# Performance work log

Hardware: AMD Instinct MI355X
Metric: run time of the kernel (lower is better)

Reference implementation:

```python
import jax, jax.numpy as jnp
import numpy as np

T, B, I, H = 129, 1024, 512, 2048


def setup_inputs() -> dict:
    key = jax.random.key(0)
    ks = jax.random.split(key, 12)
    s = 1.0 / np.sqrt(H)  # torch RNNCell/Linear default U(-1/sqrt(H), 1/sqrt(H))

    def u(k, shape):
        return jax.random.uniform(k, shape, jnp.float32, -s, s)

    x = jax.random.normal(ks[0], (T, B, I), jnp.float32)
    return {
        "x": x,
        "enc_Wih": u(ks[1], (H, I)), "enc_Whh": u(ks[2], (H, H)),
        "enc_bih": u(ks[3], (H,)),   "enc_bhh": u(ks[4], (H,)),
        "dec_Wih": u(ks[5], (H, I)), "dec_Whh": u(ks[6], (H, H)),
        "dec_bih": u(ks[7], (H,)),   "dec_bhh": u(ks[8], (H,)),
        "ro_W": u(ks[9], (I, H)),    "ro_b": u(ks[10], (I,)),
    }


def reference(x, enc_Wih, enc_Whh, enc_bih, enc_bhh,
              dec_Wih, dec_Whh, dec_bih, dec_bhh, ro_W, ro_b):
    T_, B_, I_ = x.shape
    H_ = enc_Whh.shape[0]
    k = (T_ - 3) // 2

    # ---- encode: k+2 RNNCell steps over x[0:k+2] ----
    def enc_step(h, xt):
        h = jnp.tanh(xt @ enc_Wih.T + enc_bih + h @ enc_Whh.T + enc_bhh)
        return h, None

    h0 = jnp.zeros((B_, H_), x.dtype)
    h, _ = jax.lax.scan(enc_step, h0, x[:k + 2])

    # begin_char: one-hot at index 0 (also the default fill of `outputs`)
    begin = jnp.zeros((B_, I_), x.dtype).at[:, 0].set(1.0)

    # ---- decode: k+1 steps, input is zeros (so zeros @ dec_Wih == 0) ----
    def dec_step(carry, _):
        h, done = carry
        h = jnp.tanh(dec_bih + h @ dec_Whh.T + dec_bhh)
        out = jax.nn.log_softmax(h @ ro_W.T + ro_b, axis=1)  # [B, I]
        z = (jnp.argmax(out, axis=1) == 2).astype(x.dtype)
        done = jnp.maximum(done, z)
        b = done[:, None]
        o = (1.0 - b) * out + b * begin
        return (h, done), o

    done0 = jnp.zeros((B_,), x.dtype)
    (_, _), outputs = jax.lax.scan(dec_step, (h, done0), None, length=k + 1)
    return outputs  # [k+1, B, I]
```

## Files before the change

kernel.cpp:

```cpp
#include <hip/hip_runtime.h>
#include <math.h>

constexpr int Bsz  = 1024;
constexpr int Isz  = 512;
constexpr int Hsz  = 2048;
constexpr int Tenc = 65;
constexpr int Tdec = 64;
constexpr int BI   = Bsz * Isz;
constexpr int MNh  = Bsz * Hsz;

typedef _Float16 half8 __attribute__((ext_vector_type(8)));
typedef float    f32x4 __attribute__((ext_vector_type(4)));
typedef unsigned int uint;
typedef unsigned short ushort;

__device__ inline uint pack_split(float v) {
    _Float16 a0 = (_Float16)v;
    float r = (v - (float)a0) * 4096.f;
    _Float16 a1 = (_Float16)r;
    return ((uint)__builtin_bit_cast(ushort, a1) << 16) | __builtin_bit_cast(ushort, a0);
}

struct U8 { uint4 a, b; };
__device__ inline U8 ld8(const uint* __restrict__ p) {
    U8 r; r.a = *(const uint4*)p; r.b = *(const uint4*)(p + 4); return r;
}

__device__ inline void split8(const U8& v, half8& lo, half8& hi) {
    union { uint4 u; float f[4]; } A, B;
    A.u = v.a; B.u = v.b;
    float x[8] = {A.f[0], A.f[1], A.f[2], A.f[3], B.f[0], B.f[1], B.f[2], B.f[3]};
#pragma unroll
    for (int e = 0; e < 8; ++e) {
        _Float16 a0 = (_Float16)x[e];
        float r = (x[e] - (float)a0) * 4096.f;
        lo[e] = a0; hi[e] = (_Float16)r;
    }
}

__device__ inline void unpack8(const U8& v, half8& lo, half8& hi) {
    union { uint u[4]; half8 h; } L, H;
    uint w[8] = {v.a.x, v.a.y, v.a.z, v.a.w, v.b.x, v.b.y, v.b.z, v.b.w};
#pragma unroll
    for (int q = 0; q < 4; ++q) {
        L.u[q] = __builtin_amdgcn_perm(w[2*q+1], w[2*q], 0x05040100u);
        H.u[q] = __builtin_amdgcn_perm(w[2*q+1], w[2*q], 0x07060302u);
    }
    lo = L.h; hi = H.h;
}

__device__ __forceinline__ void gll16(const uint* g, uint* l) {
    __builtin_amdgcn_global_load_lds(
        (const __attribute__((address_space(1))) void*)(uintptr_t)g,
        (__attribute__((address_space(3))) void*)(unsigned int)(uintptr_t)l,
        16, 0, 0);
}

__device__ __forceinline__ void gemm_body(
    uint* ldsA, uint* ldsB,
    const uint* A1, int K1, const uint* B1,
    const uint* A2, int K2, const uint* B2,
    float* P, int M, int N, int GM, int GN, int KS, int bid)
{
    constexpr int NV = 8;
    const int tid  = threadIdx.x;
    const int wid  = tid >> 6, lane = tid & 63;
    const int wr   = wid >> 1, wc = wid & 1;
    const int kq   = lane >> 4, lr = lane & 15;

    const int xcd = bid & 7, g = bid >> 3;
    int n_b, m_b, ks;
    const int spx = GN >> 3;
    if (spx > 0) {
        n_b = xcd * spx + (g % spx);
        int r = g / spx; m_b = r % GM; ks = r / GM;
    } else {
        const int xpn = 8 / GN;
        n_b = xcd / xpn;
        int r = g * xpn + (xcd % xpn); m_b = r % GM; ks = r / GM;
    }
    const int m0 = m_b * 128, n0 = n_b * 128;

    int offA1[4], offA2[4], offB1[4], offB2[4];
#pragma unroll
    for (int q = 0; q < 4; ++q) {
        int U = q * 256 + tid, row = U >> 3, us = U & 7;
        int u = us ^ (row & 7);
        offA1[q] = (m0 + row) * K1 + u * 4;
        offA2[q] = (m0 + row) * K2 + u * 4;
        offB1[q] = (n0 + row) * K1 + u * 4;
        offB2[q] = (n0 + row) * K2 + u * 4;
    }
    const int ldsbase = wid * 256;

    const int R1 = K1 / 32;
    const int R  = (K1 + K2) / 32;
    const int nr = R / KS;
    const int r0 = ks * nr;

    auto STAGE = [&](int r, int bi) {
        uint* Ab = ldsA + bi * 4096;
        uint* Bb = ldsB + bi * 4096;
        const bool ph1 = r < R1;
        const int kl = (ph1 ? r : r - R1) * 32;
        const uint* As = ph1 ? A1 : A2;
        const uint* Bs = ph1 ? B1 : B2;
#pragma unroll
        for (int q = 0; q < 4; ++q)
            gll16(As + (ph1 ? offA1[q] : offA2[q]) + kl, Ab + q * 1024 + ldsbase);
#pragma unroll
        for (int q = 0; q < 4; ++q)
            gll16(Bs + (ph1 ? offB1[q] : offB2[q]) + kl, Bb + q * 1024 + ldsbase);
    };

    f32x4 acc0[4][4] = {}; f32x4 acc1[4][4] = {};

    auto FRAG = [&](const uint* buf, int row, half8& lo, half8& hi) {
        const int b = row * 8, s = row & 7;
        U8 v;
        v.a = *(const uint4*)(buf + (b + ((2 * kq)     ^ s)) * 4);
        v.b = *(const uint4*)(buf + (b + ((2 * kq + 1) ^ s)) * 4);
        unpack8(v, lo, hi);
    };

    auto COMPUTE = [&](int bi) {
        const uint* Ab = ldsA + bi * 4096;
        const uint* Bb = ldsB + bi * 4096;
        half8 a0[4], a1[4];
#pragma unroll
        for (int i = 0; i < 4; ++i) FRAG(Ab, wr * 64 + i * 16 + lr, a0[i], a1[i]);
#pragma unroll
        for (int j = 0; j < 4; ++j) {
            half8 b0, b1;
            FRAG(Bb, wc * 64 + j * 16 + lr, b0, b1);
#pragma unroll
            for (int i = 0; i < 4; ++i) {
                acc0[i][j] = __builtin_amdgcn_mfma_f32_16x16x32_f16(a0[i], b0, acc0[i][j], 0, 0, 0);
                acc1[i][j] = __builtin_amdgcn_mfma_f32_16x16x32_f16(a1[i], b0, acc1[i][j], 0, 0, 0);
                acc1[i][j] = __builtin_amdgcn_mfma_f32_16x16x32_f16(a0[i], b1, acc1[i][j], 0, 0, 0);
            }
        }
    };

    STAGE(r0, 0);
    if (nr > 1) STAGE(r0 + 1, 1);
    __builtin_amdgcn_sched_barrier(0);
    if (nr > 1) asm volatile("s_waitcnt vmcnt(%0)" :: "i"(NV) : "memory");
    else        asm volatile("s_waitcnt vmcnt(0)"  ::: "memory");
    __builtin_amdgcn_s_barrier();
    __builtin_amdgcn_sched_barrier(0);

    int bi = 0;
    for (int t = 0; t < nr; ++t) {
        COMPUTE(bi);
        if (t + 1 < nr) {
            __builtin_amdgcn_sched_barrier(0);
            __builtin_amdgcn_s_barrier();
            __builtin_amdgcn_sched_barrier(0);
            if (t + 2 < nr) {
                STAGE(r0 + t + 2, bi);
                __builtin_amdgcn_sched_barrier(0);
                asm volatile("s_waitcnt vmcnt(%0)" :: "i"(NV) : "memory");
            } else {
                asm volatile("s_waitcnt vmcnt(0)" ::: "memory");
            }
            __builtin_amdgcn_s_barrier();
            __builtin_amdgcn_sched_barrier(0);
            bi ^= 1;
        }
    }

    float* Pk = P + (size_t)ks * M * N;
#pragma unroll
    for (int j = 0; j < 4; ++j) {
        const int n = n0 + wc * 64 + j * 16 + lr;
#pragma unroll
        for (int i = 0; i < 4; ++i) {
            const int mb = m0 + wr * 64 + i * 16 + kq * 4;
#pragma unroll
            for (int r = 0; r < 4; ++r)
                Pk[(size_t)(mb + r) * N + n] = acc0[i][j][r] + 0x1p-12f * acc1[i][j][r];
        }
    }
}

__global__ __launch_bounds__(256, 2) void gemm_pk4(
    const uint* __restrict__ A1, int K1, const uint* __restrict__ B1,
    const uint* __restrict__ A2, int K2, const uint* __restrict__ B2,
    float* __restrict__ P, int M, int N, int GM, int GN, int KS)
{
    __shared__ uint ldsA[2 * 4096];
    __shared__ uint ldsB[2 * 4096];
    gemm_body(ldsA, ldsB, A1, K1, B1, A2, K2, B2, P, M, N, GM, GN, KS, blockIdx.x);
}

__global__ __launch_bounds__(256, 2) void dec_work(
    const uint* __restrict__ hcur, const uint* __restrict__ pdWhh,
    const uint* __restrict__ proW,
    float* __restrict__ hparts, float* __restrict__ ropar, int doH)
{
    __shared__ uint ldsA[2 * 4096];
    __shared__ uint ldsB[2 * 4096];
    const int bid = blockIdx.x;
    if (bid < 512) {
        if (!doH) return;
        gemm_body(ldsA, ldsB, nullptr, 0, nullptr, hcur, Hsz, pdWhh,
                  hparts, Bsz, Hsz, 8, 16, 4, bid);
    } else {
        gemm_body(ldsA, ldsB, nullptr, 0, nullptr, hcur, Hsz, proW,
                  ropar, Bsz, Isz, 8, 4, 8, bid - 512);
    }
}

__device__ __forceinline__ void combine_dev(
    const float* __restrict__ P, const float* __restrict__ b1,
    const float* __restrict__ b2, uint* __restrict__ hout, int cb)
{
    const int i0 = (cb * 256 + threadIdx.x) * 8;
    float s[8];
#pragma unroll
    for (int e = 0; e < 8; ++e) s[e] = 0.f;
#pragma unroll
    for (int p = 0; p < 4; ++p) {
        float4 a = *(const float4*)(P + (size_t)p * MNh + i0);
        float4 b = *(const float4*)(P + (size_t)p * MNh + i0 + 4);
        s[0] += a.x; s[1] += a.y; s[2] += a.z; s[3] += a.w;
        s[4] += b.x; s[5] += b.y; s[6] += b.z; s[7] += b.w;
    }
    const int n = i0 & (Hsz - 1);
    uint4 oa, ob;
    oa.x = pack_split(tanhf(s[0] + b1[n+0] + b2[n+0]));
    oa.y = pack_split(tanhf(s[1] + b1[n+1] + b2[n+1]));
    oa.z = pack_split(tanhf(s[2] + b1[n+2] + b2[n+2]));
    oa.w = pack_split(tanhf(s[3] + b1[n+3] + b2[n+3]));
    ob.x = pack_split(tanhf(s[4] + b1[n+4] + b2[n+4]));
    ob.y = pack_split(tanhf(s[5] + b1[n+5] + b2[n+5]));
    ob.z = pack_split(tanhf(s[6] + b1[n+6] + b2[n+6]));
    ob.w = pack_split(tanhf(s[7] + b1[n+7] + b2[n+7]));
    *(uint4*)(hout + i0)     = oa;
    *(uint4*)(hout + i0 + 4) = ob;
}

__global__ __launch_bounds__(256) void combine_h4(
    const float* __restrict__ P, const float* __restrict__ b1,
    const float* __restrict__ b2, uint* __restrict__ hout)
{
    combine_dev(P, b1, b2, hout, blockIdx.x);
}

template<int NPART>
__device__ __forceinline__ void softmax_dev(
    const float* __restrict__ parts, const float* __restrict__ rob,
    float* __restrict__ done, float* __restrict__ out, int b)
{
    const int tid = threadIdx.x;
    const size_t S = (size_t)BI;
    const float* row = parts + (size_t)b * Isz;

    float v0, v1;
    if (NPART == 1) { v0 = row[tid]; v1 = row[tid + 256]; }
    else {
        v0 = rob[tid]; v1 = rob[tid + 256];
#pragma unroll
        for (int p = 0; p < NPART; ++p) { v0 += row[p*S + tid]; v1 += row[p*S + tid + 256]; }
    }

    float mv; int mi;
    if (v0 >= v1) { mv = v0; mi = tid; } else { mv = v1; mi = tid + 256; }
#pragma unroll
    for (int off = 32; off; off >>= 1) {
        float ov = __shfl_xor(mv, off);
        int   oi = __shfl_xor(mi, off);
        if (ov > mv || (ov == mv && oi < mi)) { mv = ov; mi = oi; }
    }
    __shared__ float smv[4];
    __shared__ int   smi[4];
    __shared__ float sdone;
    const int wid = tid >> 6, lane = tid & 63;
    if (lane == 0) { smv[wid] = mv; smi[wid] = mi; }
    __syncthreads();
    if (tid == 0) {
        for (int w = 1; w < 4; ++w)
            if (smv[w] > smv[0] || (smv[w] == smv[0] && smi[w] < smi[0])) {
                smv[0] = smv[w]; smi[0] = smi[w];
            }
        float z = (smi[0] == 2) ? 1.f : 0.f;
        float dn = fmaxf(done[b], z);
        done[b] = dn;
        sdone = dn;
    }
    __syncthreads();
    mv = smv[0];

    float s = expf(v0 - mv) + expf(v1 - mv);
#pragma unroll
    for (int off = 32; off; off >>= 1) s += __shfl_xor(s, off);
    __shared__ float ssum[4];
    if (lane == 0) ssum[wid] = s;
    __syncthreads();
    if (tid == 0) ssum[0] = ssum[0] + ssum[1] + ssum[2] + ssum[3];
    __syncthreads();
    const float ls = logf(ssum[0]);

    float* orow = out + (size_t)b * Isz;
    if (sdone > 0.5f) {
        orow[tid]       = (tid == 0) ? 1.f : 0.f;
        orow[tid + 256] = 0.f;
    } else {
        orow[tid]       = v0 - mv - ls;
        orow[tid + 256] = v1 - mv - ls;
    }
}

__global__ __launch_bounds__(256) void dec_fin(
    const float* __restrict__ hparts, const float* __restrict__ dbih,
    const float* __restrict__ dbhh, uint* __restrict__ hout,
    const float* __restrict__ ropar, const float* __restrict__ rob,
    float* __restrict__ done, float* __restrict__ out, int doH)
{
    const int bid = blockIdx.x;
    if (bid < 1024) {
        if (doH) combine_dev(hparts, dbih, dbhh, hout, bid);
    } else {
        softmax_dev<8>(ropar, rob, done, out, bid - 1024);
    }
}

__global__ __launch_bounds__(256) void logsoftmax_done1(
    const float* __restrict__ logits, const float* __restrict__ rob,
    float* __restrict__ done, float* __restrict__ out)
{
    softmax_dev<1>(logits, rob, done, out, blockIdx.x);
}

__global__ __launch_bounds__(256) void split_pack_k(
    const float* __restrict__ s, uint* __restrict__ d, int n)
{
    for (int i = blockIdx.x * 256 + threadIdx.x; i < n; i += gridDim.x * 256)
        d[i] = pack_split(s[i]);
}

#define SWZ(row, kk) (((row) * 4 + ((kk) ^ (((row) >> 1) & 3))) * 8)

template<int BM, int BN, int WR, int WC, int MP, int NP, bool TANH, bool PACKOUT>
__global__ __launch_bounds__(WR*WC*64) void gemm_sp(
    const float* __restrict__ A1, int K1, const void* __restrict__ B1,
    const uint*  __restrict__ A2, int K2, const void* __restrict__ B2,
    int b_f32,
    const float* __restrict__ bias1, const float* __restrict__ bias2,
    void* __restrict__ C, int M, int N)
{
    constexpr int NT  = WR * WC * 64;
    constexpr int AUP = BM * 4 / NT;
    constexpr int BUP = BN * 4 / NT;

    __shared__ __align__(16) _Float16 As0[BM*32], As1[BM*32];
    __shared__ __align__(16) _Float16 Bs0[BN*32], Bs1[BN*32];

    const int tid  = threadIdx.x;
    const int wid  = tid >> 6, lane = tid & 63;
    const int wrow = wid / WC, wcol = wid % WC;
    const int kq   = lane >> 4, lr = lane & 15;
    const int m0   = blockIdx.y * BM;
    const int n0   = blockIdx.x * BN;

    int aum[AUP], auk[AUP]; _Float16 *aw0[AUP], *aw1[AUP];
#pragma unroll
    for (int p = 0; p < AUP; ++p) {
        int u = tid + p * NT; aum[p] = u >> 2; auk[p] = u & 3;
        int o = SWZ(aum[p], auk[p]); aw0[p] = As0 + o; aw1[p] = As1 + o;
    }
    int bun[BUP], buk[BUP]; _Float16 *bw0[BUP], *bw1[BUP];
#pragma unroll
    for (int p = 0; p < BUP; ++p) {
        int u = tid + p * NT; bun[p] = u >> 2; buk[p] = u & 3;
        int o = SWZ(bun[p], buk[p]); bw0[p] = Bs0 + o; bw1[p] = Bs1 + o;
    }
    int aoff[MP], boff[NP];
#pragma unroll
    for (int i = 0; i < MP; ++i) { int m = wrow*(MP*16) + i*16 + lr; aoff[i] = SWZ(m, kq); }
#pragma unroll
    for (int j = 0; j < NP; ++j) { int n = wcol*(NP*16) + j*16 + lr; boff[j] = SWZ(n, kq); }

    f32x4 acc0[MP][NP] = {}; f32x4 acc1[MP][NP] = {};

    const int R = (K1 + K2) / 32;

    auto issue = [&](int rd, U8* aR, U8* bR) {
        const bool ph1 = (rd * 32) < K1;
        const int  kl  = ph1 ? rd * 32 : rd * 32 - K1;
        const int  Ka  = ph1 ? K1 : K2;
        const uint* Ap = ph1 ? (const uint*)A1 : A2;
        const uint* Bp = (const uint*)(ph1 ? B1 : B2);
#pragma unroll
        for (int p = 0; p < AUP; ++p)
            aR[p] = ld8(Ap + (size_t)(m0 + aum[p]) * Ka + kl + auk[p] * 8);
#pragma unroll
        for (int p = 0; p < BUP; ++p)
            bR[p] = ld8(Bp + (size_t)(n0 + bun[p]) * Ka + kl + buk[p] * 8);
    };

    auto stage = [&](U8* aR, U8* bR, bool aF32) {
#pragma unroll
        for (int p = 0; p < AUP; ++p) {
            half8 lo, hi;
            if (aF32) split8(aR[p], lo, hi); else unpack8(aR[p], lo, hi);
            *(half8*)aw0[p] = lo; *(half8*)aw1[p] = hi;
        }
#pragma unroll
        for (int p = 0; p < BUP; ++p) {
            half8 lo, hi;
            if (b_f32) split8(bR[p], lo, hi); else unpack8(bR[p], lo, hi);
            *(half8*)bw0[p] = lo; *(half8*)bw1[p] = hi;
        }
    };

    auto compute = [&]() {
        half8 a0[MP], a1[MP], b0[NP], b1[NP];
#pragma unroll
        for (int i = 0; i < MP; ++i) {
            a0[i] = *(const half8*)(As0 + aoff[i]);
            a1[i] = *(const half8*)(As1 + aoff[i]);
        }
#pragma unroll
        for (int j = 0; j < NP; ++j) {
            b0[j] = *(const half8*)(Bs0 + boff[j]);
            b1[j] = *(const half8*)(Bs1 + boff[j]);
        }
#pragma unroll
        for (int i = 0; i < MP; ++i)
#pragma unroll
            for (int j = 0; j < NP; ++j) {
                acc0[i][j] = __builtin_amdgcn_mfma_f32_16x16x32_f16(a0[i], b0[j], acc0[i][j], 0, 0, 0);
                acc1[i][j] = __builtin_amdgcn_mfma_f32_16x16x32_f16(a1[i], b0[j], acc1[i][j], 0, 0, 0);
                acc1[i][j] = __builtin_amdgcn_mfma_f32_16x16x32_f16(a0[i], b1[j], acc1[i][j], 0, 0, 0);
            }
    };

    U8 aA[AUP], bA[BUP], aB[AUP], bB[BUP];
    issue(0, aA, bA);
    for (int rd = 0; rd < R; rd += 2) {
        if (rd + 1 < R) issue(rd + 1, aB, bB);
        stage(aA, bA, (rd * 32) < K1);
        __syncthreads();
        compute();
        __syncthreads();
        if (rd + 1 < R) {
            if (rd + 2 < R) issue(rd + 2, aA, bA);
            stage(aB, bB, ((rd + 1) * 32) < K1);
            __syncthreads();
            compute();
            __syncthreads();
        }
    }

#pragma unroll
    for (int j = 0; j < NP; ++j) {
        const int n = n0 + wcol*(NP*16) + j*16 + lr;
        float bb = bias1 ? bias1[n] : 0.f;
        if (bias2) bb += bias2[n];
#pragma unroll
        for (int i = 0; i < MP; ++i) {
            const int mb = m0 + wrow*(MP*16) + i*16 + kq*4;
#pragma unroll
            for (int r = 0; r < 4; ++r) {
                float val = acc0[i][j][r] + 0x1p-12f * acc1[i][j][r] + bb;
                if (TANH) val = tanhf(val);
                if (PACKOUT)
                    ((uint*)C)[(size_t)(mb + r) * N + n] = pack_split(val);
                else
                    ((float*)C)[(size_t)(mb + r) * N + n] = val;
            }
        }
    }
}

extern "C" void kernel_launch(void* const* d_in, const int* in_sizes, int n_in,
                              void* d_out, int out_size, void* d_ws, size_t ws_size,
                              hipStream_t stream)
{
    const float* x    = (const float*)d_in[0];
    const float* eWih = (const float*)d_in[1];
    const float* eWhh = (const float*)d_in[2];
    const float* ebih = (const float*)d_in[3];
    const float* ebhh = (const float*)d_in[4];
    const float* dWhh = (const float*)d_in[6];
    const float* dbih = (const float*)d_in[7];
    const float* dbhh = (const float*)d_in[8];
    const float* roW  = (const float*)d_in[9];
    const float* rob  = (const float*)d_in[10];
    float* out = (float*)d_out;

    const size_t sz_pWih = (size_t)Hsz * Isz * 4;
    const size_t sz_pWhh = (size_t)Hsz * Hsz * 4;
    const size_t sz_proW = (size_t)Isz * Hsz * 4;
    const size_t sz_h    = (size_t)MNh * 4;
    const size_t sz_hp   = (size_t)4 * MNh * 4;
    const size_t sz_rp   = (size_t)8 * BI * 4;
    const size_t sz_done = (size_t)Bsz * 4;
    const size_t sz_px2  = (size_t)Tenc * BI * 4;
    const size_t sz_slot = (size_t)BI * 4;

    const size_t base = sz_pWih + 2*sz_pWhh + sz_proW + 2*sz_h + sz_hp + sz_rp + sz_done;
    const int mode = (ws_size >= base + sz_px2) ? 2
                   : (ws_size >= base + sz_slot) ? 1 : 0;

    char* ws = (char*)d_ws;

    if (mode >= 1) {
        size_t off = 0;
        uint* pWih   = (uint*)(ws + off); off += sz_pWih;
        uint* pWhh   = (uint*)(ws + off); off += sz_pWhh;
        uint* pdWhh  = (uint*)(ws + off); off += sz_pWhh;
        uint* proW   = (uint*)(ws + off); off += sz_proW;
        uint* hA     = (uint*)(ws + off); off += sz_h;
        uint* hB     = (uint*)(ws + off); off += sz_h;
        float* hparts= (float*)(ws + off); off += sz_hp;
        float* ropar = (float*)(ws + off); off += sz_rp;
        float* done  = (float*)(ws + off); off += sz_done;
        uint* px     = (uint*)(ws + off);

        split_pack_k<<<dim3(1024), dim3(256), 0, stream>>>(eWih, pWih,  Hsz*Isz);
        split_pack_k<<<dim3(2048), dim3(256), 0, stream>>>(eWhh, pWhh,  Hsz*Hsz);
        split_pack_k<<<dim3(2048), dim3(256), 0, stream>>>(dWhh, pdWhh, Hsz*Hsz);
        split_pack_k<<<dim3(1024), dim3(256), 0, stream>>>(roW,  proW,  Isz*Hsz);
        if (mode == 2)
            split_pack_k<<<dim3(2048), dim3(256), 0, stream>>>(x, px, Tenc*BI);

        hipMemsetAsync(hA,   0, sz_h,    stream);
        hipMemsetAsync(done, 0, sz_done, stream);

        uint* h[2] = { hA, hB };
        int cur = 0;
        for (int t = 0; t < Tenc; ++t) {
            const uint* xs;
            if (mode == 2) xs = px + (size_t)t * BI;
            else {
                split_pack_k<<<dim3(512), dim3(256), 0, stream>>>(
                    x + (size_t)t * BI, px, BI);
                xs = px;
            }
            gemm_pk4<<<dim3(512), dim3(256), 0, stream>>>(
                xs, Isz, pWih, h[cur], Hsz, pWhh,
                hparts, Bsz, Hsz, 8, 16, 4);
            combine_h4<<<dim3(1024), dim3(256), 0, stream>>>(
                hparts, ebih, ebhh, h[cur ^ 1]);
            cur ^= 1;
        }
        gemm_pk4<<<dim3(512), dim3(256), 0, stream>>>(
            nullptr, 0, nullptr, h[cur], Hsz, pdWhh,
            hparts, Bsz, Hsz, 8, 16, 4);
        combine_h4<<<dim3(1024), dim3(256), 0, stream>>>(
            hparts, dbih, dbhh, h[cur ^ 1]);
        cur ^= 1;
        for (int t = 0; t < Tdec; ++t) {
            const int doH = (t + 1 < Tdec) ? 1 : 0;
            dec_work<<<dim3(768), dim3(256), 0, stream>>>(
                h[cur], pdWhh, proW, hparts, ropar, doH);
            dec_fin<<<dim3(2048), dim3(256), 0, stream>>>(
                hparts, dbih, dbhh, h[cur ^ 1],
                ropar, rob, done, out + (size_t)t * BI, doH);
            cur ^= 1;
        }
        return;
    }

    {
        const size_t sz_lg = (size_t)BI * 4;
        size_t off = 0;
        uint*  hA     = (uint*)(ws + off); off += sz_h;
        uint*  hB     = (uint*)(ws + off); off += sz_h;
        float* logits = (float*)(ws + off); off += sz_lg;
        float* done   = (float*)(ws + off);

        hipMemsetAsync(hA, 0, sz_h, stream);
        hipMemsetAsync(done, 0, sz_done, stream);

        uint* h[2] = { hA, hB };
        const dim3 blk(256);
        const dim3 grid_h(Hsz / 128, Bsz / 64);
        const dim3 grid_ro(Isz / 64, Bsz / 64);

        int cur = 0;
        for (int t = 0; t < Tenc; ++t) {
            gemm_sp<64, 128, 2, 2, 2, 4, true, true><<<grid_h, blk, 0, stream>>>(
                x + (size_t)t * BI, Isz, eWih,
                h[cur], Hsz, eWhh, 1,
                ebih, ebhh, h[cur ^ 1], Bsz, Hsz);
            cur ^= 1;
        }
        for (int t = 0; t < Tdec; ++t) {
            gemm_sp<64, 128, 2, 2, 2, 4, true, true><<<grid_h, blk, 0, stream>>>(
                nullptr, 0, nullptr, h[cur], Hsz, dWhh, 1,
                dbih, dbhh, h[cur ^ 1], Bsz, Hsz);
            cur ^= 1;
            gemm_sp<64, 64, 2, 2, 2, 2, false, false><<<grid_ro, blk, 0, stream>>>(
                nullptr, 0, nullptr, h[cur], Hsz, roW, 1,
                rob, nullptr, logits, Bsz, Isz);
            logsoftmax_done1<<<dim3(Bsz), dim3(256), 0, stream>>>(
                logits, rob, done, out + (size_t)t * BI);
        }
    }
}
```

Measured before the change: 6.739 ms.

## Defer decoder log-softmax into next step's GEMM launch with double-buffered partials

Moves the decoder's log-softmax/done step for step t-1 into the dec_work kernel of step t as extra blocks that process four rows each. The readout partials are double-buffered so this work can overlap the next step's GEMMs, and the old dec_fin is replaced by a plain combine kernel. A final sm_final kernel handles the last step's softmax. The four weight pack launches and two memsets are also merged into one prep kernel; the cost is a second readout partial buffer and a tighter workspace threshold.

```diff
diff --git a/kernel.cpp b/kernel.cpp
--- a/kernel.cpp
+++ b/kernel.cpp
@@ -194,60 +194,6 @@
     gemm_body(ldsA, ldsB, A1, K1, B1, A2, K2, B2, P, M, N, GM, GN, KS, blockIdx.x);
 }
 
-__global__ __launch_bounds__(256, 2) void dec_work(
-    const uint* __restrict__ hcur, const uint* __restrict__ pdWhh,
-    const uint* __restrict__ proW,
-    float* __restrict__ hparts, float* __restrict__ ropar, int doH)
-{
-    __shared__ uint ldsA[2 * 4096];
-    __shared__ uint ldsB[2 * 4096];
-    const int bid = blockIdx.x;
-    if (bid < 512) {
-        if (!doH) return;
-        gemm_body(ldsA, ldsB, nullptr, 0, nullptr, hcur, Hsz, pdWhh,
-                  hparts, Bsz, Hsz, 8, 16, 4, bid);
-    } else {
-        gemm_body(ldsA, ldsB, nullptr, 0, nullptr, hcur, Hsz, proW,
-                  ropar, Bsz, Isz, 8, 4, 8, bid - 512);
-    }
-}
-
-__device__ __forceinline__ void combine_dev(
-    const float* __restrict__ P, const float* __restrict__ b1,
-    const float* __restrict__ b2, uint* __restrict__ hout, int cb)
-{
-    const int i0 = (cb * 256 + threadIdx.x) * 8;
-    float s[8];
-#pragma unroll
-    for (int e = 0; e < 8; ++e) s[e] = 0.f;
-#pragma unroll
-    for (int p = 0; p < 4; ++p) {
-        float4 a = *(const float4*)(P + (size_t)p * MNh + i0);
-        float4 b = *(const float4*)(P + (size_t)p * MNh + i0 + 4);
-        s[0] += a.x; s[1] += a.y; s[2] += a.z; s[3] += a.w;
-        s[4] += b.x; s[5] += b.y; s[6] += b.z; s[7] += b.w;
-    }
-    const int n = i0 & (Hsz - 1);
-    uint4 oa, ob;
-    oa.x = pack_split(tanhf(s[0] + b1[n+0] + b2[n+0]));
-    oa.y = pack_split(tanhf(s[1] + b1[n+1] + b2[n+1]));
-    oa.z = pack_split(tanhf(s[2] + b1[n+2] + b2[n+2]));
-    oa.w = pack_split(tanhf(s[3] + b1[n+3] + b2[n+3]));
-    ob.x = pack_split(tanhf(s[4] + b1[n+4] + b2[n+4]));
-    ob.y = pack_split(tanhf(s[5] + b1[n+5] + b2[n+5]));
-    ob.z = pack_split(tanhf(s[6] + b1[n+6] + b2[n+6]));
-    ob.w = pack_split(tanhf(s[7] + b1[n+7] + b2[n+7]));
-    *(uint4*)(hout + i0)     = oa;
-    *(uint4*)(hout + i0 + 4) = ob;
-}
-
-__global__ __launch_bounds__(256) void combine_h4(
-    const float* __restrict__ P, const float* __restrict__ b1,
-    const float* __restrict__ b2, uint* __restrict__ hout)
-{
-    combine_dev(P, b1, b2, hout, blockIdx.x);
-}
-
 template<int NPART>
 __device__ __forceinline__ void softmax_dev(
     const float* __restrict__ parts, const float* __restrict__ rob,
@@ -312,25 +258,101 @@
     }
 }
 
-__global__ __launch_bounds__(256) void dec_fin(
-    const float* __restrict__ hparts, const float* __restrict__ dbih,
-    const float* __restrict__ dbhh, uint* __restrict__ hout,
+template<int NPART>
+__device__ __forceinline__ void sm4_dev(
+    const float* __restrict__ parts, const float* __restrict__ rob,
+    float* __restrict__ done, float* __restrict__ out, int row0)
+{
+    for (int rr = 0; rr < 4; ++rr) {
+        __syncthreads();
+        softmax_dev<NPART>(parts, rob, done, out, row0 + rr);
+    }
+}
+
+__global__ __launch_bounds__(256, 2) void dec_work(
+    const uint* __restrict__ hcur, const uint* __restrict__ pdWhh,
+    const uint* __restrict__ proW,
+    float* __restrict__ hparts, float* __restrict__ ropar_cur,
+    const float* __restrict__ ropar_prev, const float* __restrict__ rob,
+    float* __restrict__ done, float* __restrict__ out_prev,
+    int doH, int doSM)
+{
+    __shared__ uint ldsA[2 * 4096];
+    __shared__ uint ldsB[2 * 4096];
+    const int bid = blockIdx.x;
+    if (bid < 512) {
+        if (!doH) return;
+        gemm_body(ldsA, ldsB, nullptr, 0, nullptr, hcur, Hsz, pdWhh,
+                  hparts, Bsz, Hsz, 8, 16, 4, bid);
+    } else if (bid < 768) {
+        gemm_body(ldsA, ldsB, nullptr, 0, nullptr, hcur, Hsz, proW,
+                  ropar_cur, Bsz, Isz, 8, 4, 8, bid - 512);
+    } else {
+        if (!doSM) return;
+        sm4_dev<8>(ropar_prev, rob, done, out_prev, (bid - 768) * 4);
+    }
+}
+
+__global__ __launch_bounds__(256) void sm_final(
     const float* __restrict__ ropar, const float* __restrict__ rob,
-    float* __restrict__ done, float* __restrict__ out, int doH)
-{
-    const int bid = blockIdx.x;
-    if (bid < 1024) {
-        if (doH) combine_dev(hparts, dbih, dbhh, hout, bid);
-    } else {
-        softmax_dev<8>(ropar, rob, done, out, bid - 1024);
-    }
-}
-
-__global__ __launch_bounds__(256) void logsoftmax_done1(
-    const float* __restrict__ logits, const float* __restrict__ rob,
     float* __restrict__ done, float* __restrict__ out)
 {
-    softmax_dev<1>(logits, rob, done, out, blockIdx.x);
+    sm4_dev<8>(ropar, rob, done, out, blockIdx.x * 4);
+}
+
+__device__ __forceinline__ void combine_dev(
+    const float* __restrict__ P, const float* __restrict__ b1,
+    const float* __restrict__ b2, uint* __restrict__ hout, int cb)
+{
+    const int i0 = (cb * 256 + threadIdx.x) * 8;
+    float s[8];
+#pragma unroll
+    for (int e = 0; e < 8; ++e) s[e] = 0.f;
+#pragma unroll
+    for (int p = 0; p < 4; ++p) {
+        float4 a = *(const float4*)(P + (size_t)p * MNh + i0);
+        float4 b = *(const float4*)(P + (size_t)p * MNh + i0 + 4);
+        s[0] += a.x; s[1] += a.y; s[2] += a.z; s[3] += a.w;
+        s[4] += b.x; s[5] += b.y; s[6] += b.z; s[7] += b.w;
+    }
+    const int n = i0 & (Hsz - 1);
+    uint4 oa, ob;
+    oa.x = pack_split(tanhf(s[0] + b1[n+0] + b2[n+0]));
+    oa.y = pack_split(tanhf(s[1] + b1[n+1] + b2[n+1]));
+    oa.z = pack_split(tanhf(s[2] + b1[n+2] + b2[n+2]));
+    oa.w = pack_split(tanhf(s[3] + b1[n+3] + b2[n+3]));
+    ob.x = pack_split(tanhf(s[4] + b1[n+4] + b2[n+4]));
+    ob.y = pack_split(tanhf(s[5] + b1[n+5] + b2[n+5]));
+    ob.z = pack_split(tanhf(s[6] + b1[n+6] + b2[n+6]));
+    ob.w = pack_split(tanhf(s[7] + b1[n+7] + b2[n+7]));
+    *(uint4*)(hout + i0)     = oa;
+    *(uint4*)(hout + i0 + 4) = ob;
+}
+
+__global__ __launch_bounds__(256) void combine_h4(
+    const float* __restrict__ P, const float* __restrict__ b1,
+    const float* __restrict__ b2, uint* __restrict__ hout)
+{
+    combine_dev(P, b1, b2, hout, blockIdx.x);
+}
+
+__global__ __launch_bounds__(256) void prep_all(
+    const float* __restrict__ eWih, uint* __restrict__ pWih,
+    const float* __restrict__ eWhh, uint* __restrict__ pWhh,
+    const float* __restrict__ dWhh, uint* __restrict__ pdWhh,
+    const float* __restrict__ roW,  uint* __restrict__ proW,
+    const float* __restrict__ x,    uint* __restrict__ px, int nx,
+    uint* __restrict__ hA, float* __restrict__ done)
+{
+    const int stride = gridDim.x * 256;
+    const int gid = blockIdx.x * 256 + threadIdx.x;
+    for (int i = gid; i < Hsz*Isz; i += stride) pWih[i]  = pack_split(eWih[i]);
+    for (int i = gid; i < Hsz*Hsz; i += stride) pWhh[i]  = pack_split(eWhh[i]);
+    for (int i = gid; i < Hsz*Hsz; i += stride) pdWhh[i] = pack_split(dWhh[i]);
+    for (int i = gid; i < Isz*Hsz; i += stride) proW[i]  = pack_split(roW[i]);
+    for (int i = gid; i < nx;      i += stride) px[i]    = pack_split(x[i]);
+    for (int i = gid; i < MNh;     i += stride) hA[i]    = 0u;
+    for (int i = gid; i < Bsz;     i += stride) done[i]  = 0.f;
 }
 
 __global__ __launch_bounds__(256) void split_pack_k(
@@ -475,6 +497,13 @@
     }
 }
 
+__global__ __launch_bounds__(256) void logsoftmax_done1(
+    const float* __restrict__ logits, const float* __restrict__ rob,
+    float* __restrict__ done, float* __restrict__ out)
+{
+    softmax_dev<1>(logits, rob, done, out, blockIdx.x);
+}
+
 extern "C" void kernel_launch(void* const* d_in, const int* in_sizes, int n_in,
                               void* d_out, int out_size, void* d_ws, size_t ws_size,
                               hipStream_t stream)
@@ -501,7 +530,7 @@
     const size_t sz_px2  = (size_t)Tenc * BI * 4;
     const size_t sz_slot = (size_t)BI * 4;
 
-    const size_t base = sz_pWih + 2*sz_pWhh + sz_proW + 2*sz_h + sz_hp + sz_rp + sz_done;
+    const size_t base = sz_pWih + 2*sz_pWhh + sz_proW + 2*sz_h + sz_hp + 2*sz_rp + sz_done;
     const int mode = (ws_size >= base + sz_px2) ? 2
                    : (ws_size >= base + sz_slot) ? 1 : 0;
 
@@ -516,20 +545,16 @@
         uint* hA     = (uint*)(ws + off); off += sz_h;
         uint* hB     = (uint*)(ws + off); off += sz_h;
         float* hparts= (float*)(ws + off); off += sz_hp;
-        float* ropar = (float*)(ws + off); off += sz_rp;
+        float* ropA  = (float*)(ws + off); off += sz_rp;
+        float* ropB  = (float*)(ws + off); off += sz_rp;
         float* done  = (float*)(ws + off); off += sz_done;
         uint* px     = (uint*)(ws + off);
 
-        split_pack_k<<<dim3(1024), dim3(256), 0, stream>>>(eWih, pWih,  Hsz*Isz);
-        split_pack_k<<<dim3(2048), dim3(256), 0, stream>>>(eWhh, pWhh,  Hsz*Hsz);
-        split_pack_k<<<dim3(2048), dim3(256), 0, stream>>>(dWhh, pdWhh, Hsz*Hsz);
-        split_pack_k<<<dim3(1024), dim3(256), 0, stream>>>(roW,  proW,  Isz*Hsz);
-        if (mode == 2)
-            split_pack_k<<<dim3(2048), dim3(256), 0, stream>>>(x, px, Tenc*BI);
-
-        hipMemsetAsync(hA,   0, sz_h,    stream);
-        hipMemsetAsync(done, 0, sz_done, stream);
-
+        prep_all<<<dim3(2048), dim3(256), 0, stream>>>(
+            eWih, pWih, eWhh, pWhh, dWhh, pdWhh, roW, proW,
+            x, px, (mode == 2) ? Tenc * BI : 0, hA, done);
+
+        float* rop[2] = { ropA, ropB };
         uint* h[2] = { hA, hB };
         int cur = 0;
         for (int t = 0; t < Tenc; ++t) {
@@ -554,14 +579,19 @@
             hparts, dbih, dbhh, h[cur ^ 1]);
         cur ^= 1;
         for (int t = 0; t < Tdec; ++t) {
-            const int doH = (t + 1 < Tdec) ? 1 : 0;
-            dec_work<<<dim3(768), dim3(256), 0, stream>>>(
-                h[cur], pdWhh, proW, hparts, ropar, doH);
-            dec_fin<<<dim3(2048), dim3(256), 0, stream>>>(
-                hparts, dbih, dbhh, h[cur ^ 1],
-                ropar, rob, done, out + (size_t)t * BI, doH);
+            const int doH  = (t + 1 < Tdec) ? 1 : 0;
+            const int doSM = (t > 0) ? 1 : 0;
+            dec_work<<<dim3(1024), dim3(256), 0, stream>>>(
+                h[cur], pdWhh, proW, hparts, rop[t & 1],
+                rop[(t & 1) ^ 1], rob, done,
+                doSM ? out + (size_t)(t - 1) * BI : out, doH, doSM);
+            if (doH)
+                combine_h4<<<dim3(1024), dim3(256), 0, stream>>>(
+                    hparts, dbih, dbhh, h[cur ^ 1]);
             cur ^= 1;
         }
+        sm_final<<<dim3(256), dim3(256), 0, stream>>>(
+            rop[(Tdec - 1) & 1], rob, done, out + (size_t)(Tdec - 1) * BI);
         return;
     }
 
```

Result: slower. 7.007 ms (+4.0%).
